# Optimization experiments

Measured on AMD Instinct MI355X. Metric: run time of the kernel, lower is better.

## Reference

```python
import jax, jax.numpy as jnp
import numpy as np

NUM_HEADS = 16
NUM_KV_HEADS = 4
HEAD_DIM = 256
ROPE_THETA = 10000.0


def _rope(x, position_ids):
    # x: [B, H, S, D], position_ids: [B, S]
    d = x.shape[-1]
    inv_freq = 1.0 / (ROPE_THETA ** (jnp.arange(0, d, 2, dtype=jnp.float32) / d))  # [D/2]
    freqs = position_ids.astype(jnp.float32)[:, :, None] * inv_freq[None, None, :]  # [B, S, D/2]
    emb = jnp.concatenate([freqs, freqs], axis=-1)  # [B, S, D]
    cos = jnp.cos(emb)[:, None, :, :]
    sin = jnp.sin(emb)[:, None, :, :]
    x1, x2 = jnp.split(x, 2, axis=-1)
    rot = jnp.concatenate([-x2, x1], axis=-1)
    return x * cos + rot * sin


def setup_inputs() -> dict:
    key = jax.random.key(0)
    k1, k2, k3, k4, k5 = jax.random.split(key, 5)
    B, S, H = 2, 2048, 2048
    hidden_states = jax.random.normal(k1, (B, S, H), dtype=jnp.float32)
    position_ids = jnp.broadcast_to(jnp.arange(S, dtype=jnp.int32)[None, :], (B, S))
    scale = 1.0 / np.sqrt(H)
    wq = jax.random.normal(k2, (H, NUM_HEADS * HEAD_DIM), dtype=jnp.float32) * scale
    wk = jax.random.normal(k3, (H, NUM_KV_HEADS * HEAD_DIM), dtype=jnp.float32) * scale
    wv = jax.random.normal(k4, (H, NUM_KV_HEADS * HEAD_DIM), dtype=jnp.float32) * scale
    wo = jax.random.normal(k5, (NUM_HEADS * HEAD_DIM, H), dtype=jnp.float32) * (1.0 / np.sqrt(NUM_HEADS * HEAD_DIM))
    return {"hidden_states": hidden_states, "position_ids": position_ids,
            "wq": wq, "wk": wk, "wv": wv, "wo": wo}


def reference(hidden_states, position_ids, wq, wk, wv, wo):
    B, S, H = hidden_states.shape
    groups = NUM_HEADS // NUM_KV_HEADS
    # QKV projections -> [B, heads, S, D]
    q = (hidden_states @ wq).reshape(B, S, NUM_HEADS, HEAD_DIM).transpose(0, 2, 1, 3)
    k = (hidden_states @ wk).reshape(B, S, NUM_KV_HEADS, HEAD_DIM).transpose(0, 2, 1, 3)
    v = (hidden_states @ wv).reshape(B, S, NUM_KV_HEADS, HEAD_DIM).transpose(0, 2, 1, 3)
    q = _rope(q, position_ids)
    k = _rope(k, position_ids)
    # GQA without materializing repeated K/V: group query heads per kv head
    qg = q.reshape(B, NUM_KV_HEADS, groups, S, HEAD_DIM)
    scale = 1.0 / jnp.sqrt(jnp.asarray(HEAD_DIM, dtype=q.dtype))
    scores = jnp.einsum('bkgqd,bkvd->bkgqv', qg, k) * scale  # [B, KV, G, S, S]
    causal = jnp.tril(jnp.ones((S, S), dtype=bool))
    scores = jnp.where(causal[None, None, None, :, :], scores, jnp.finfo(scores.dtype).min)
    probs = jax.nn.softmax(scores, axis=-1)
    out = jnp.einsum('bkgqv,bkvd->bkgqd', probs, v)  # [B, KV, G, S, D]
    out = out.reshape(B, NUM_HEADS, S, HEAD_DIM).transpose(0, 2, 1, 3).reshape(B, S, NUM_HEADS * HEAD_DIM)
    return out @ wo
```

## Files before the change

kernel.cpp:

```cpp
#include <hip/hip_runtime.h>

typedef unsigned short u16;
typedef __bf16 bf16_t;
typedef bf16_t bf16x8 __attribute__((ext_vector_type(8)));
typedef float f32x4 __attribute__((ext_vector_type(4)));
typedef float f32x16 __attribute__((ext_vector_type(16)));

#define LOG2E 1.4426950408889634f

__device__ __forceinline__ u16 f2bf(float f) {
  union { float f; unsigned u; } c; c.f = f;
  unsigned r = c.u + 0x7fffu + ((c.u >> 16) & 1u);
  return (u16)(r >> 16);
}
__device__ __forceinline__ float bf2f(u16 u) {
  union { unsigned u; float f; } c; c.u = ((unsigned)u) << 16;
  return c.f;
}

__device__ __forceinline__ void gload16(const void* g, void* l) {
  __builtin_amdgcn_global_load_lds(
      (const __attribute__((address_space(1))) unsigned int*)g,
      (__attribute__((address_space(3))) unsigned int*)l, 16, 0, 0);
}

__device__ __forceinline__ unsigned cvtpk(float lo, float hi) {
  unsigned r;
  asm("v_cvt_pk_bf16_f32 %0, %1, %2" : "=v"(r) : "v"(lo), "v"(hi));
  return r;
}
__device__ __forceinline__ void swap32(unsigned& a, unsigned& b) {
  asm("v_permlane32_swap_b32 %0, %1" : "+v"(a), "+v"(b));
}

#define MFMA16(a, b, c) __builtin_amdgcn_mfma_f32_16x16x32_bf16((a), (b), (c), 0, 0, 0)
#define MFMA32(a, b, c) __builtin_amdgcn_mfma_f32_32x32x16_bf16((a), (b), (c), 0, 0, 0)


__global__ __launch_bounds__(256) void k_convert_f32_bf16(const float* __restrict__ in,
                                                          u16* __restrict__ out, int n4) {
  int i = blockIdx.x * 256 + threadIdx.x;
  if (i >= n4) return;
  float4 v = ((const float4*)in)[i];
  ushort4 o;
  o.x = f2bf(v.x); o.y = f2bf(v.y); o.z = f2bf(v.z); o.w = f2bf(v.w);
  ((ushort4*)out)[i] = o;
}

__global__ __launch_bounds__(256) void k_transpose_f32_bf16(const float* __restrict__ in,
                                                            u16* __restrict__ out, int R, int C) {
  __shared__ float tile[32][33];
  int tx = threadIdx.x, ty = threadIdx.y;
  int bx = blockIdx.x * 32, by = blockIdx.y * 32;
#pragma unroll
  for (int i = 0; i < 4; i++)
    tile[ty + i * 8][tx] = in[(size_t)(by + ty + i * 8) * C + bx + tx];
  __syncthreads();
#pragma unroll
  for (int i = 0; i < 4; i++)
    out[(size_t)(bx + ty + i * 8) * R + by + tx] = f2bf(tile[tx][ty + i * 8]);
}

__global__ __launch_bounds__(256) void k_transpose_bf16(const u16* __restrict__ in,
                                                        u16* __restrict__ out, int R, int C) {
  __shared__ u16 tile[32][33];
  int tx = threadIdx.x, ty = threadIdx.y;
  int bx = blockIdx.x * 32, by = blockIdx.y * 32;
#pragma unroll
  for (int i = 0; i < 4; i++)
    tile[ty + i * 8][tx] = in[(size_t)(by + ty + i * 8) * C + bx + tx];
  __syncthreads();
#pragma unroll
  for (int i = 0; i < 4; i++)
    out[(size_t)(bx + ty + i * 8) * R + by + tx] = tile[tx][ty + i * 8];
}

__global__ __launch_bounds__(256) void k_rope(u16* __restrict__ x, const int* __restrict__ pos,
                                              int nh_mask, int nh_shift, int width) {
  int idx = blockIdx.x * 256 + threadIdx.x;
  int i = idx & 127;
  int h = (idx >> 7) & nh_mask;
  int row = idx >> (7 + nh_shift);
  int p = pos[row];
  float f = (float)p * exp2f((float)i * (-13.287712379549449f / 128.f));
  float sn, cs;
  sincosf(f, &sn, &cs);
  size_t base = (size_t)row * width + h * 256 + i;
  float x1 = bf2f(x[base]), x2 = bf2f(x[base + 128]);
  x[base] = f2bf(x1 * cs - x2 * sn);
  x[base + 128] = f2bf(x2 * cs + x1 * sn);
}


template <int OUT_BF16>
__global__ __launch_bounds__(256) void k_gemm_bt(const u16* __restrict__ A,
                                                 const u16* __restrict__ Bt,
                                                 void* __restrict__ C, int M, int N, int K) {
  __shared__ u16 As[128 * 64];
  __shared__ u16 Bs[128 * 64];
  const int tid = threadIdx.x;
  const int lane = tid & 63;
  const int w = tid >> 6;
  const int l15 = lane & 15, l4 = lane >> 4;
  const int wr = w >> 1, wc = w & 1;
  const int bx = blockIdx.x, by = blockIdx.y;

  f32x4 acc[4][4];
#pragma unroll
  for (int a = 0; a < 4; a++)
#pragma unroll
    for (int b2 = 0; b2 < 4; b2++) acc[a][b2] = (f32x4){0.f, 0.f, 0.f, 0.f};

  const u16* Abase = A + (size_t)by * 128 * K;
  const u16* Bbase = Bt + (size_t)bx * 128 * K;

  for (int kk = 0; kk < K; kk += 64) {
    __syncthreads();
#pragma unroll
    for (int j = 0; j < 4; j++) {
      int ci = w * 256 + j * 64 + lane;
      int row = ci >> 3, c = ci & 7;
      gload16(Abase + (size_t)row * K + kk + c * 8, (char*)As + ci * 16);
      gload16(Bbase + (size_t)row * K + kk + c * 8, (char*)Bs + ci * 16);
    }
    __syncthreads();
#pragma unroll
    for (int kc = 0; kc < 2; kc++) {
      int kb = kc * 64 + l4 * 16;
      bf16x8 av[4], bv[4];
#pragma unroll
      for (int mt = 0; mt < 4; mt++)
        av[mt] = *(const bf16x8*)((const char*)As + (wr * 64 + mt * 16 + l15) * 128 + kb);
#pragma unroll
      for (int nt = 0; nt < 4; nt++)
        bv[nt] = *(const bf16x8*)((const char*)Bs + (wc * 64 + nt * 16 + l15) * 128 + kb);
#pragma unroll
      for (int mt = 0; mt < 4; mt++)
#pragma unroll
        for (int nt = 0; nt < 4; nt++) acc[mt][nt] = MFMA16(av[mt], bv[nt], acc[mt][nt]);
    }
  }
#pragma unroll
  for (int mt = 0; mt < 4; mt++) {
#pragma unroll
    for (int nt = 0; nt < 4; nt++) {
      int col = bx * 128 + wc * 64 + nt * 16 + l15;
#pragma unroll
      for (int r = 0; r < 4; r++) {
        int row = by * 128 + wr * 64 + mt * 16 + l4 * 4 + r;
        if (OUT_BF16)
          ((u16*)C)[(size_t)row * N + col] = f2bf(acc[mt][nt][r]);
        else
          ((float*)C)[(size_t)row * N + col] = acc[mt][nt][r];
      }
    }
  }
}


__shared__ __align__(16) u16 aK0[8192];
__shared__ __align__(16) u16 aK1[8192];
__shared__ __align__(16) u16 aV0[8192];
__shared__ __align__(16) u16 aV1[8192];

__global__ __launch_bounds__(256, 2) void k_attn(const u16* __restrict__ Q,
                                                 const u16* __restrict__ Kb,
                                                 const u16* __restrict__ Vt,
                                                 u16* __restrict__ AO) {
  const int tid = threadIdx.x, lane = tid & 63, w = tid >> 6;
  const int r31 = lane & 31, hi = lane >> 5;

  const int flat = blockIdx.x;
  const int r = flat & 7;
  const int idx = flat >> 3;
  const int b = r >> 2, kv = r & 3;
  const int half = idx >> 5, j = idx & 31;
  const int qb = half ? 15 - (j >> 1) : (j >> 1);
  const int h = kv * 4 + (j & 1) + 2 * half;

  bf16x8 qreg[16];
  {
    const u16* qp = Q + (size_t)(b * 2048 + qb * 128 + w * 32 + r31) * 4096 + h * 256 + hi * 8;
#pragma unroll
    for (int kc = 0; kc < 16; kc++) qreg[kc] = *(const bf16x8*)(qp + kc * 16);
  }

  f32x16 o[8];
#pragma unroll
  for (int df = 0; df < 8; df++)
#pragma unroll
    for (int jj = 0; jj < 16; jj++) o[df][jj] = 0.f;
  float mrow = -3e38f, lrow = 0.f;

  const int nt = 4 * qb + 4;
  const int tlim = 4 * qb + w;
  const int qloc = qb * 128 + w * 32 + r31;
  const u16* Kbase = Kb + (size_t)(b * 2048) * 2048 + kv * 256;
  const u16* Vbase = Vt + (size_t)(kv * 256) * 4096 + b * 2048;

  int kfix[4], vfix[4];
#pragma unroll
  for (int jj = 0; jj < 4; jj++) {
    int ci = jj * 256 + tid;
    int krow = ci >> 5, kc = ci & 31;
    int kcg = (kc & 24) | ((kc ^ krow) & 7);
    kfix[jj] = krow * 2048 + kcg * 8;
    int vrow = ci >> 2, vc = ci & 3;
    int vg = (vc - (vrow >> 1)) & 3;
    vfix[jj] = vrow * 4096 + vg * 8;
  }
  int koff = 0, voff = 0;

  auto STAGE = [&](u16* Kd, u16* Vd) {
#pragma unroll
    for (int jj = 0; jj < 4; jj++)
      gload16(Kbase + kfix[jj] + koff, (char*)Kd + (jj * 256 + tid) * 16);
#pragma unroll
    for (int jj = 0; jj < 4; jj++)
      gload16(Vbase + vfix[jj] + voff, (char*)Vd + (jj * 256 + tid) * 16);
    koff += 32 * 2048;
    voff += 32;
  };

  auto COMPUTE = [&](int t, const u16* Kc, const u16* Vc) {
    f32x16 s;
#pragma unroll
    for (int jj = 0; jj < 16; jj++) s[jj] = 0.f;
#pragma unroll
    for (int kc = 0; kc < 16; kc++) {
      int ch = kc * 2 + hi;
      int cs = (ch & 24) | ((ch ^ r31) & 7);
      bf16x8 kf = *(const bf16x8*)((const char*)Kc + r31 * 512 + cs * 16);
      s = MFMA32(kf, qreg[kc], s);
    }

    const float C = 0.0625f * LOG2E;
    float z[16];
#pragma unroll
    for (int jj = 0; jj < 16; jj++) z[jj] = s[jj] * C;
    if (t == tlim) {
#pragma unroll
      for (int jj = 0; jj < 16; jj++) {
        int kvg = t * 32 + (jj & 3) + 8 * (jj >> 2) + 4 * hi;
        if (kvg > qloc) z[jj] = -1e30f;
      }
    }

    float m0 = z[0];
#pragma unroll
    for (int jj = 1; jj < 16; jj++) m0 = fmaxf(m0, z[jj]);
    m0 = fmaxf(m0, __shfl_xor(m0, 32));
    if (__any(m0 > mrow + 11.54f)) {
      float mn = fmaxf(mrow, m0);
      float alpha = exp2f(mrow - mn);
      mrow = mn;
      lrow *= alpha;
#pragma unroll
      for (int jj = 0; jj < 16; jj++) {
        float a = __shfl(alpha, (jj & 3) + 8 * (jj >> 2) + 4 * hi);
#pragma unroll
        for (int df = 0; df < 8; df++) o[df][jj] *= a;
      }
    }
    float sum = 0.f;
#pragma unroll
    for (int jj = 0; jj < 16; jj++) {
      z[jj] = exp2f(z[jj] - mrow);
      sum += z[jj];
    }
    sum += __shfl_xor(sum, 32);
    lrow += sum;

    unsigned a0 = cvtpk(z[0], z[1]), a2 = cvtpk(z[4], z[5]);
    swap32(a0, a2);
    unsigned a1 = cvtpk(z[2], z[3]), a3 = cvtpk(z[6], z[7]);
    swap32(a1, a3);
    unsigned b0 = cvtpk(z[8], z[9]), b2 = cvtpk(z[12], z[13]);
    swap32(b0, b2);
    unsigned b1 = cvtpk(z[10], z[11]), b3 = cvtpk(z[14], z[15]);
    swap32(b1, b3);
    union UU { unsigned u[4]; bf16x8 v; };
    UU ua; ua.u[0] = a0; ua.u[1] = a1; ua.u[2] = a2; ua.u[3] = a3;
    UU ub; ub.u[0] = b0; ub.u[1] = b1; ub.u[2] = b2; ub.u[3] = b3;
    bf16x8 pa0 = ua.v, pa1 = ub.v;

#pragma unroll
    for (int df = 0; df < 8; df++) {
      int vr = df * 32 + r31;
      int c0 = (hi + (vr >> 1)) & 3;
      int c1 = (2 + hi + (vr >> 1)) & 3;
      bf16x8 v0 = *(const bf16x8*)((const char*)Vc + vr * 64 + c0 * 16);
      bf16x8 v1 = *(const bf16x8*)((const char*)Vc + vr * 64 + c1 * 16);
      o[df] = MFMA32(pa0, v0, o[df]);
      o[df] = MFMA32(pa1, v1, o[df]);
    }
  };

  STAGE(aK0, aV0);
  __syncthreads();

  for (int t = 0; t < nt; t += 2) {
    STAGE(aK1, aV1);
    if (t <= tlim) COMPUTE(t, aK0, aV0);
    __syncthreads();
    if (t + 2 < nt) STAGE(aK0, aV0);
    if (t + 1 <= tlim) COMPUTE(t + 1, aK1, aV1);
    __syncthreads();
  }

  float rl = 1.f / lrow;
  size_t rowbase = (size_t)(b * 2048 + qb * 128 + w * 32);
#pragma unroll
  for (int jj = 0; jj < 16; jj++) {
    float rr = __shfl(rl, (jj & 3) + 8 * (jj >> 2) + 4 * hi);
    int qr = (jj & 3) + 8 * (jj >> 2) + 4 * hi;
#pragma unroll
    for (int df = 0; df < 8; df++)
      AO[(rowbase + qr) * 4096 + h * 256 + df * 32 + r31] = f2bf(o[df][jj] * rr);
  }
}


#define OFF_XB   0u
#define OFF_WQT  16777216u
#define OFF_WKVT 33554432u
#define OFF_WOT  41943040u
#define OFF_QB   58720256u
#define OFF_KVB  92274688u
#define OFF_VT   109051904u
#define OFF_AO   0u

extern "C" void kernel_launch(void* const* d_in, const int* in_sizes, int n_in,
                              void* d_out, int out_size, void* d_ws, size_t ws_size,
                              hipStream_t stream) {
  const float* hs = (const float*)d_in[0];
  const int* pos = (const int*)d_in[1];
  const float* wq = (const float*)d_in[2];
  const float* wk = (const float*)d_in[3];
  const float* wv = (const float*)d_in[4];
  const float* wo = (const float*)d_in[5];
  float* out = (float*)d_out;
  char* ws = (char*)d_ws;

  u16* Xb   = (u16*)(ws + OFF_XB);
  u16* Wqt  = (u16*)(ws + OFF_WQT);
  u16* Wkvt = (u16*)(ws + OFF_WKVT);
  u16* Wot  = (u16*)(ws + OFF_WOT);
  u16* Qb   = (u16*)(ws + OFF_QB);
  u16* KVb  = (u16*)(ws + OFF_KVB);
  u16* Vt   = (u16*)(ws + OFF_VT);
  u16* AO   = (u16*)(ws + OFF_AO);

  dim3 tb(32, 8);

  k_convert_f32_bf16<<<8192, 256, 0, stream>>>(hs, Xb, 2097152);
  k_transpose_f32_bf16<<<dim3(128, 64), tb, 0, stream>>>(wq, Wqt, 2048, 4096);
  k_transpose_f32_bf16<<<dim3(32, 64), tb, 0, stream>>>(wk, Wkvt, 2048, 1024);
  k_transpose_f32_bf16<<<dim3(32, 64), tb, 0, stream>>>(wv, Wkvt + 1024 * 2048, 2048, 1024);
  k_transpose_f32_bf16<<<dim3(64, 128), tb, 0, stream>>>(wo, Wot, 4096, 2048);

  k_gemm_bt<1><<<dim3(32, 32), 256, 0, stream>>>(Xb, Wqt, Qb, 4096, 4096, 2048);
  k_gemm_bt<1><<<dim3(16, 32), 256, 0, stream>>>(Xb, Wkvt, KVb, 4096, 2048, 2048);

  k_rope<<<32768, 256, 0, stream>>>(Qb, pos, 15, 4, 4096);
  k_rope<<<8192, 256, 0, stream>>>(KVb, pos, 3, 2, 2048);

  k_transpose_bf16<<<dim3(32, 128), tb, 0, stream>>>(KVb + 1024, Vt, 4096, 2048);

  k_attn<<<dim3(512), 256, 0, stream>>>(Qb, KVb, Vt, AO);

  k_gemm_bt<0><<<dim3(16, 32), 256, 0, stream>>>(AO, Wot, out, 4096, 2048, 4096);
}
```

Measured before the change: 506.0 us.

## Fuse Q/K/V projections into one 256x256-tile GEMM over concatenated weights

```diff
diff --git a/kernel.cpp b/kernel.cpp
--- a/kernel.cpp
+++ b/kernel.cpp
@@ -7,6 +7,7 @@
 typedef float f32x16 __attribute__((ext_vector_type(16)));
 
 #define LOG2E 1.4426950408889634f
+#define QKVS 6144
 
 __device__ __forceinline__ u16 f2bf(float f) {
   union { float f; unsigned u; } c; c.f = f;
@@ -158,13 +159,123 @@
 }
 
 
+__global__ __launch_bounds__(512, 1) void k_gemm256(const u16* __restrict__ A,
+                                                    const u16* __restrict__ Bt,
+                                                    u16* __restrict__ C, int N, int K) {
+  extern __shared__ char smem[];
+  const int tid = threadIdx.x;
+  const int lane = tid & 63, w = tid >> 6;
+  const int l15 = lane & 15, l4 = lane >> 4;
+  const int wr = w >> 2, wc = w & 3;
+  const int bx = blockIdx.x, by = blockIdx.y;
+  const int NT = K >> 6;
+
+  const u16* Ab = A + (size_t)(by * 256) * K;
+  const u16* Bb = Bt + (size_t)(bx * 256) * K;
+
+  int srcoff[2], dstoff[2];
+#pragma unroll
+  for (int rr = 0; rr < 2; rr++) {
+    int ci = rr * 512 + tid;
+    int lc = ci ^ (((ci >> 5) & 1) << 1);
+    int kc = lc >> 9, row = (lc >> 2) & 127, g2 = lc & 3;
+    srcoff[rr] = row * K + kc * 32 + g2 * 8;
+    dstoff[rr] = ci * 16;
+  }
+
+  auto SH = [&](int Tg, int halfidx) {
+    const u16* base = (halfidx < 2) ? (Ab + (size_t)(halfidx * 128) * K)
+                                    : (Bb + (size_t)((halfidx - 2) * 128) * K);
+    char* dst = smem + (Tg & 1) * 65536 + halfidx * 16384;
+    int kk = Tg * 64;
+#pragma unroll
+    for (int rr = 0; rr < 2; rr++)
+      gload16(base + srcoff[rr] + kk, dst + dstoff[rr]);
+  };
+
+  auto lda = [&](int c, int kc, int mrow4) -> bf16x8 {
+    int L = kc * 8192 + (mrow4 * 16 + l15) * 64 + l4 * 16;
+    int P = L ^ (((L >> 9) & 1) << 5);
+    return *(const bf16x8*)(smem + c * 65536 + wr * 16384 + P);
+  };
+  auto ldb = [&](int c, int kc, int j) -> bf16x8 {
+    int L = kc * 8192 + ((wc & 1) * 64 + j * 16 + l15) * 64 + l4 * 16;
+    int P = L ^ (((L >> 9) & 1) << 5);
+    return *(const bf16x8*)(smem + c * 65536 + 32768 + (wc >> 1) * 16384 + P);
+  };
+
+  f32x4 acc[8][4];
+#pragma unroll
+  for (int i = 0; i < 8; i++)
+#pragma unroll
+    for (int j = 0; j < 4; j++) acc[i][j] = (f32x4){0.f, 0.f, 0.f, 0.f};
+
+  SH(0, 0); SH(0, 1); SH(0, 2); SH(0, 3);
+  SH(1, 2); SH(1, 3);
+  asm volatile("s_waitcnt vmcnt(4)" ::: "memory");
+  __builtin_amdgcn_s_barrier();
+  asm volatile("" ::: "memory");
+
+  bf16x8 bv[2][4];
+  for (int T = 0; T < NT; ++T) {
+    const int c = T & 1;
+#pragma unroll
+    for (int q = 0; q < 4; q++) {
+      const int kc = q & 1, mh = q >> 1;
+      bf16x8 av[4];
+      if (q < 2) {
+#pragma unroll
+        for (int j = 0; j < 4; j++) bv[kc][j] = ldb(c, kc, j);
+      }
+#pragma unroll
+      for (int ii = 0; ii < 4; ii++) av[ii] = lda(c, kc, mh * 4 + ii);
+      if (q == 0)      { if (T + 1 < NT) SH(T + 1, 0); }
+      else if (q == 1) { if (T + 1 < NT) SH(T + 1, 1); }
+      else if (q == 2) { if (T + 2 < NT) SH(T + 2, 2); }
+      else             { if (T + 2 < NT) SH(T + 2, 3); }
+      if (q == 3) {
+        if (T < NT - 2)       asm volatile("s_waitcnt vmcnt(4)" ::: "memory");
+        else if (T == NT - 2) asm volatile("s_waitcnt vmcnt(0)" ::: "memory");
+      }
+      asm volatile("" ::: "memory");
+      __builtin_amdgcn_s_barrier();
+      asm volatile("" ::: "memory");
+      asm volatile("s_waitcnt lgkmcnt(0)" ::: "memory");
+      __builtin_amdgcn_sched_barrier(0);
+      __builtin_amdgcn_s_setprio(1);
+#pragma unroll
+      for (int ii = 0; ii < 4; ii++)
+#pragma unroll
+        for (int j = 0; j < 4; j++)
+          acc[mh * 4 + ii][j] = MFMA16(av[ii], bv[kc][j], acc[mh * 4 + ii][j]);
+      __builtin_amdgcn_s_setprio(0);
+      asm volatile("" ::: "memory");
+      __builtin_amdgcn_s_barrier();
+      asm volatile("" ::: "memory");
+    }
+  }
+
+#pragma unroll
+  for (int i = 0; i < 8; i++) {
+#pragma unroll
+    for (int j = 0; j < 4; j++) {
+      int col = bx * 256 + wc * 64 + j * 16 + l15;
+#pragma unroll
+      for (int r = 0; r < 4; r++) {
+        int row = by * 256 + wr * 128 + i * 16 + l4 * 4 + r;
+        C[(size_t)row * N + col] = f2bf(acc[i][j][r]);
+      }
+    }
+  }
+}
+
+
 __shared__ __align__(16) u16 aK0[8192];
 __shared__ __align__(16) u16 aK1[8192];
 __shared__ __align__(16) u16 aV0[8192];
 __shared__ __align__(16) u16 aV1[8192];
 
-__global__ __launch_bounds__(256, 2) void k_attn(const u16* __restrict__ Q,
-                                                 const u16* __restrict__ Kb,
+__global__ __launch_bounds__(256, 2) void k_attn(const u16* __restrict__ QKV,
                                                  const u16* __restrict__ Vt,
                                                  u16* __restrict__ AO) {
   const int tid = threadIdx.x, lane = tid & 63, w = tid >> 6;
@@ -180,7 +291,7 @@
 
   bf16x8 qreg[16];
   {
-    const u16* qp = Q + (size_t)(b * 2048 + qb * 128 + w * 32 + r31) * 4096 + h * 256 + hi * 8;
+    const u16* qp = QKV + (size_t)(b * 2048 + qb * 128 + w * 32 + r31) * QKVS + h * 256 + hi * 8;
 #pragma unroll
     for (int kc = 0; kc < 16; kc++) qreg[kc] = *(const bf16x8*)(qp + kc * 16);
   }
@@ -195,7 +306,7 @@
   const int nt = 4 * qb + 4;
   const int tlim = 4 * qb + w;
   const int qloc = qb * 128 + w * 32 + r31;
-  const u16* Kbase = Kb + (size_t)(b * 2048) * 2048 + kv * 256;
+  const u16* Kbase = QKV + (size_t)(b * 2048) * QKVS + 4096 + kv * 256;
   const u16* Vbase = Vt + (size_t)(kv * 256) * 4096 + b * 2048;
 
   int kfix[4], vfix[4];
@@ -204,7 +315,7 @@
     int ci = jj * 256 + tid;
     int krow = ci >> 5, kc = ci & 31;
     int kcg = (kc & 24) | ((kc ^ krow) & 7);
-    kfix[jj] = krow * 2048 + kcg * 8;
+    kfix[jj] = krow * QKVS + kcg * 8;
     int vrow = ci >> 2, vc = ci & 3;
     int vg = (vc - (vrow >> 1)) & 3;
     vfix[jj] = vrow * 4096 + vg * 8;
@@ -218,7 +329,7 @@
 #pragma unroll
     for (int jj = 0; jj < 4; jj++)
       gload16(Vbase + vfix[jj] + voff, (char*)Vd + (jj * 256 + tid) * 16);
-    koff += 32 * 2048;
+    koff += 32 * QKVS;
     voff += 32;
   };
 
@@ -312,23 +423,21 @@
   size_t rowbase = (size_t)(b * 2048 + qb * 128 + w * 32);
 #pragma unroll
   for (int jj = 0; jj < 16; jj++) {
-    float rr = __shfl(rl, (jj & 3) + 8 * (jj >> 2) + 4 * hi);
+    float rr2 = __shfl(rl, (jj & 3) + 8 * (jj >> 2) + 4 * hi);
     int qr = (jj & 3) + 8 * (jj >> 2) + 4 * hi;
 #pragma unroll
     for (int df = 0; df < 8; df++)
-      AO[(rowbase + qr) * 4096 + h * 256 + df * 32 + r31] = f2bf(o[df][jj] * rr);
-  }
-}
-
-
-#define OFF_XB   0u
-#define OFF_WQT  16777216u
-#define OFF_WKVT 33554432u
-#define OFF_WOT  41943040u
-#define OFF_QB   58720256u
-#define OFF_KVB  92274688u
-#define OFF_VT   109051904u
-#define OFF_AO   0u
+      AO[(rowbase + qr) * 4096 + h * 256 + df * 32 + r31] = f2bf(o[df][jj] * rr2);
+  }
+}
+
+
+#define OFF_AO    0u
+#define OFF_XB    0u
+#define OFF_WQKVT 16777216u
+#define OFF_VT    33554432u
+#define OFF_WOT   41943040u
+#define OFF_QKV   58720256u
 
 extern "C" void kernel_launch(void* const* d_in, const int* in_sizes, int n_in,
                               void* d_out, int out_size, void* d_ws, size_t ws_size,
@@ -342,32 +451,31 @@
   float* out = (float*)d_out;
   char* ws = (char*)d_ws;
 
-  u16* Xb   = (u16*)(ws + OFF_XB);
-  u16* Wqt  = (u16*)(ws + OFF_WQT);
-  u16* Wkvt = (u16*)(ws + OFF_WKVT);
-  u16* Wot  = (u16*)(ws + OFF_WOT);
-  u16* Qb   = (u16*)(ws + OFF_QB);
-  u16* KVb  = (u16*)(ws + OFF_KVB);
-  u16* Vt   = (u16*)(ws + OFF_VT);
-  u16* AO   = (u16*)(ws + OFF_AO);
+  u16* Xb    = (u16*)(ws + OFF_XB);
+  u16* Wqkvt = (u16*)(ws + OFF_WQKVT);
+  u16* Vt    = (u16*)(ws + OFF_VT);
+  u16* Wot   = (u16*)(ws + OFF_WOT);
+  u16* QKV   = (u16*)(ws + OFF_QKV);
+  u16* AO    = (u16*)(ws + OFF_AO);
 
   dim3 tb(32, 8);
 
   k_convert_f32_bf16<<<8192, 256, 0, stream>>>(hs, Xb, 2097152);
-  k_transpose_f32_bf16<<<dim3(128, 64), tb, 0, stream>>>(wq, Wqt, 2048, 4096);
-  k_transpose_f32_bf16<<<dim3(32, 64), tb, 0, stream>>>(wk, Wkvt, 2048, 1024);
-  k_transpose_f32_bf16<<<dim3(32, 64), tb, 0, stream>>>(wv, Wkvt + 1024 * 2048, 2048, 1024);
+  k_transpose_f32_bf16<<<dim3(128, 64), tb, 0, stream>>>(wq, Wqkvt, 2048, 4096);
+  k_transpose_f32_bf16<<<dim3(32, 64), tb, 0, stream>>>(wk, Wqkvt + 4096 * 2048, 2048, 1024);
+  k_transpose_f32_bf16<<<dim3(32, 64), tb, 0, stream>>>(wv, Wqkvt + 5120 * 2048, 2048, 1024);
   k_transpose_f32_bf16<<<dim3(64, 128), tb, 0, stream>>>(wo, Wot, 4096, 2048);
 
-  k_gemm_bt<1><<<dim3(32, 32), 256, 0, stream>>>(Xb, Wqt, Qb, 4096, 4096, 2048);
-  k_gemm_bt<1><<<dim3(16, 32), 256, 0, stream>>>(Xb, Wkvt, KVb, 4096, 2048, 2048);
-
-  k_rope<<<32768, 256, 0, stream>>>(Qb, pos, 15, 4, 4096);
-  k_rope<<<8192, 256, 0, stream>>>(KVb, pos, 3, 2, 2048);
-
-  k_transpose_bf16<<<dim3(32, 128), tb, 0, stream>>>(KVb + 1024, Vt, 4096, 2048);
-
-  k_attn<<<dim3(512), 256, 0, stream>>>(Qb, KVb, Vt, AO);
+  (void)hipFuncSetAttribute((const void*)k_gemm256,
+                            hipFuncAttributeMaxDynamicSharedMemorySize, 131072);
+  k_gemm256<<<dim3(24, 16), 512, 131072, stream>>>(Xb, Wqkvt, QKV, 6144, 2048);
+
+  k_rope<<<32768, 256, 0, stream>>>(QKV, pos, 15, 4, QKVS);
+  k_rope<<<8192, 256, 0, stream>>>(QKV + 4096, pos, 3, 2, QKVS);
+
+  k_transpose_bf16<<<dim3(32, 128), tb, 0, stream>>>(QKV + 5120, Vt, 4096, QKVS);
+
+  k_attn<<<dim3(512), 256, 0, stream>>>(QKV, Vt, AO);
 
   k_gemm_bt<0><<<dim3(16, 32), 256, 0, stream>>>(AO, Wot, out, 4096, 2048, 4096);
 }
```

After: 479.4 us. -5.2%, faster.
